# Optimization experiments

Hardware: AMD Instinct MI355X
Metric: run time of the kernel (lower is better)

Reference implementation:

```python
import jax, jax.numpy as jnp
import numpy as np

S, P, D, KH, KW = 1, 1, 1, 3, 3  # stride, padding, dilation, kernel
EPS = 1e-5


def _conv(x, w, b):
    y = jax.lax.conv_general_dilated(
        x, w, (S, S), [(P, P), (P, P)], rhs_dilation=(D, D),
        dimension_numbers=('NCHW', 'OIHW', 'NCHW'))
    return y + b[None, :, None, None]


def _deform_conv(x, offset, mask, w, b):
    # torchvision deform_conv2d v2 semantics: offset layout [B, 2*K, Ho, Wo]
    # with (dy, dx) interleaved per kernel tap; bilinear sampling w/ zero pad.
    B, C, H, W = x.shape
    K = KH * KW
    Ho, Wo = offset.shape[2], offset.shape[3]
    ki, kj = jnp.meshgrid(jnp.arange(KH), jnp.arange(KW), indexing='ij')
    ki = ki.reshape(K).astype(offset.dtype)
    kj = kj.reshape(K).astype(offset.dtype)
    base_y = (jnp.arange(Ho, dtype=offset.dtype) * S - P)[None, None, :, None] + (ki * D)[None, :, None, None]
    base_x = (jnp.arange(Wo, dtype=offset.dtype) * S - P)[None, None, None, :] + (kj * D)[None, :, None, None]
    off = offset.reshape(B, K, 2, Ho, Wo)
    py = base_y + off[:, :, 0]  # [B,K,Ho,Wo]
    px = base_x + off[:, :, 1]
    y0 = jnp.floor(py)
    x0 = jnp.floor(px)
    ly = py - y0
    lx = px - x0
    y0i = y0.astype(jnp.int32)
    x0i = x0.astype(jnp.int32)

    def corner(iy, ix, wgt):
        valid = (iy >= 0) & (iy < H) & (ix >= 0) & (ix < W)
        iyc = jnp.clip(iy, 0, H - 1)
        ixc = jnp.clip(ix, 0, W - 1)
        # gather -> [B, C, K, Ho, Wo]
        v = jax.vmap(lambda img, a, bb: img[:, a, bb])(x, iyc, ixc)
        return v * (wgt * valid)[:, None]

    val = (corner(y0i, x0i, (1 - ly) * (1 - lx))
           + corner(y0i, x0i + 1, (1 - ly) * lx)
           + corner(y0i + 1, x0i, ly * (1 - lx))
           + corner(y0i + 1, x0i + 1, ly * lx))
    val = val * mask[:, None]  # modulation, mask: [B,K,Ho,Wo]
    O = w.shape[0]
    out = jnp.einsum('bckhw,ock->bohw', val, w.reshape(O, C, K))
    return out + b[None, :, None, None]


def setup_inputs() -> dict:
    key = jax.random.key(0)
    ks = jax.random.split(key, 8)
    B, Cin, H, W = 16, 64, 64, 64
    Cout, K = 128, KH * KW
    fan = Cin * K
    x = jax.random.normal(ks[0], (B, Cin, H, W), jnp.float32)
    w_p = jax.random.normal(ks[1], (2 * K, Cin, KH, KW), jnp.float32) * 0.02
    b_p = jax.random.normal(ks[2], (2 * K,), jnp.float32) * 0.01
    w_m = jax.random.normal(ks[3], (K, Cin, KH, KW), jnp.float32) * 0.02
    b_m = jax.random.normal(ks[4], (K,), jnp.float32) * 0.01
    w_d = jax.random.normal(ks[5], (Cout, Cin, KH, KW), jnp.float32) / np.sqrt(fan)
    b_d = jax.random.normal(ks[6], (Cout,), jnp.float32) * 0.01
    gamma = jnp.ones((Cout,), jnp.float32)
    beta = jnp.zeros((Cout,), jnp.float32)
    return {"x": x, "w_p": w_p, "b_p": b_p, "w_m": w_m, "b_m": b_m,
            "w_d": w_d, "b_d": b_d, "gamma": gamma, "beta": beta}


def reference(x, w_p, b_p, w_m, b_m, w_d, b_d, gamma, beta):
    offset = _conv(x, w_p, b_p)                 # [B, 2K, Ho, Wo]
    mask = jax.nn.sigmoid(_conv(x, w_m, b_m))   # [B, K, Ho, Wo]
    y = _deform_conv(x, offset, mask, w_d, b_d)
    # BatchNorm2d (training-mode batch stats, biased variance, eps=1e-5)
    mu = y.mean(axis=(0, 2, 3), keepdims=True)
    var = y.var(axis=(0, 2, 3), keepdims=True)
    yn = (y - mu) * jax.lax.rsqrt(var + EPS)
    yn = yn * gamma[None, :, None, None] + beta[None, :, None, None]
    return jax.nn.gelu(yn, approximate=False)  # nn.GELU default = exact erf
```

## Files before the change

kernel.cpp:

```cpp
#include <hip/hip_runtime.h>
#include <math.h>

#define BB 16
#define CIN 64
#define HH 64
#define WW 64
#define COUT 128
#define HW 4096
#define CK 576
#define CKP 584

typedef __attribute__((ext_vector_type(8))) short short8;
typedef __attribute__((ext_vector_type(4))) float f32x4;

#define WT_OFF    0
#define WPM_OFF   36864
#define XH_OFF    46080
#define SAB_OFF   8434688
#define STAT_OFF  8434944

__device__ __forceinline__ short f2bf(float f) {
    union { float f; unsigned u; } cv; cv.f = f;
    unsigned u = cv.u;
    unsigned r = (u + 0x7fffu + ((u >> 16) & 1u)) >> 16;
    return (short)r;
}
__device__ __forceinline__ float bf2f(short s) {
    union { unsigned u; float f; } cv;
    cv.u = ((unsigned)(unsigned short)s) << 16;
    return cv.f;
}
__device__ __forceinline__ unsigned cvt_pk_bf16(float lo, float hi) {
    unsigned r;
    asm("v_cvt_pk_bf16_f32 %0, %1, %2" : "=v"(r) : "v"(lo), "v"(hi));
    return r;
}

__global__ __launch_bounds__(256) void k_nhwc(const float* __restrict__ x,
                                              short* __restrict__ xh) {
    __shared__ float t[64][65];
    const int blk  = blockIdx.x;
    const int b    = blk >> 6;
    const int pos0 = (blk & 63) << 6;
    const int a    = threadIdx.x & 63;
    const int q    = threadIdx.x >> 6;
#pragma unroll
    for (int i = 0; i < 16; ++i) {
        int c = i * 4 + q;
        t[c][a] = x[((size_t)(b * CIN + c)) * HW + pos0 + a];
    }
    __syncthreads();
#pragma unroll
    for (int i = 0; i < 16; ++i) {
        int p = i * 4 + q;
        xh[((size_t)b * HW + pos0 + p) * CIN + a] = f2bf(t[a][p]);
    }
}

__global__ __launch_bounds__(256) void k_pack(const float* __restrict__ wd,
                                              const float* __restrict__ wp,
                                              const float* __restrict__ wm,
                                              short* __restrict__ wt2,
                                              short* __restrict__ wpm2) {
    int i = blockIdx.x * 256 + threadIdx.x;
    if (i < 18 * 128 * 32) {
        int kc  = i >> 12;
        int rem = i & 4095;
        int co  = rem >> 5;
        int kl  = rem & 31;
        int kk  = kc * 32 + kl;
        int k   = kk >> 6;
        int c   = kk & 63;
        wt2[i] = f2bf(wd[co * CK + c * 9 + k]);
        return;
    }
    i -= 18 * 128 * 32;
    if (i < 18 * 32 * 32) {
        int kc  = i >> 10;
        int rem = i & 1023;
        int t   = rem >> 5;
        int kl  = rem & 31;
        int kk  = kc * 32 + kl;
        int k   = kk >> 6;
        int c   = kk & 63;
        float v = 0.f;
        if (t < 18)      v = wp[t * CK + c * 9 + k];
        else if (t < 27) v = wm[(t - 18) * CK + c * 9 + k];
        wpm2[i] = f2bf(v);
    }
}

__device__ __forceinline__ short8 conv_a(const short* __restrict__ xb,
                                         int ho, int wo, int lk, int kc) {
    const int k  = kc >> 1;
    const int c0 = (kc & 1) * 32 + lk * 8;
    const int yy = ho - 1 + k / 3;
    const int xx = wo - 1 + k % 3;
    const bool valid = ((unsigned)yy < 64u) & ((unsigned)xx < 64u);
    const int yyc = min(max(yy, 0), 63);
    const int xxc = min(max(xx, 0), 63);
    short8 a = *(const short8*)&xb[(((yyc << 6) + xxc) << 6) + c0];
    if (!valid) a = (short8)0;
    return a;
}

#define MPB 32
__global__ __launch_bounds__(512) void k_deform(const short* __restrict__ xh,
                                                const short* __restrict__ wt2,
                                                const short* __restrict__ wpm2,
                                                const float* __restrict__ bp,
                                                const float* __restrict__ bm,
                                                const float* __restrict__ bd,
                                                float* __restrict__ y,
                                                float* __restrict__ gstat) {
    __shared__ short     val[MPB * CKP];
    __shared__ float     s_pm2[2][32][MPB];
    __shared__ unsigned  s_yx[MPB * 9];
    __shared__ _Float16  s_wh[MPB * 9 * 4];

    const int bid  = blockIdx.x;
    const int swz  = (bid & 7) * 256 + (bid >> 3);
    const int pos0 = swz * MPB;
    const int b   = pos0 >> 12;
    const int ho  = (pos0 >> 6) & 63;
    const int wo0 = pos0 & 63;
    const int tid = threadIdx.x;
    const int wv   = tid >> 6;
    const int lane = tid & 63;
    const int l15  = lane & 15;
    const int lk   = lane >> 4;

    const short* xb = xh + (size_t)b * HW * CIN;

    {
        const int mw = wv & 1;
        const int nw = (wv >> 1) & 1;
        const int kh = wv >> 2;
        const int t  = nw * 16 + l15;
        const short* wr = wpm2 + t * 32 + lk * 8;
        const int wo = wo0 + mw * 16 + l15;
        f32x4 acc = (f32x4)(0.f);
#pragma unroll
        for (int kc = kh * 9; kc < kh * 9 + 9; ++kc) {
            short8 a  = conv_a(xb, ho, wo, lk, kc);
            short8 bf = *(const short8*)&wr[kc * 1024];
            acc = __builtin_amdgcn_mfma_f32_16x16x32_bf16(a, bf, acc, 0, 0, 0);
        }
#pragma unroll
        for (int j = 0; j < 4; ++j)
            s_pm2[kh][t][mw * 16 + lk * 4 + j] = acc[j];
    }
    __syncthreads();

    if (tid < MPB * 9) {
        int k = tid >> 5;
        int p = tid & 31;
        int wo = wo0 + p;
        float dy = s_pm2[0][2 * k    ][p] + s_pm2[1][2 * k    ][p] + bp[2 * k];
        float dx = s_pm2[0][2 * k + 1][p] + s_pm2[1][2 * k + 1][p] + bp[2 * k + 1];
        float mm = s_pm2[0][18 + k   ][p] + s_pm2[1][18 + k   ][p] + bm[k];
        float m  = 1.f / (1.f + expf(-mm));
        float py = (float)(ho - 1 + k / 3) + dy;
        float px = (float)(wo - 1 + k % 3) + dx;
        float fy = floorf(py), fx = floorf(px);
        float ly = py - fy, lx = px - fx;
        int y0 = (int)fy, x0 = (int)fx;
        int y1 = y0 + 1, x1 = x0 + 1;
        float vy0 = ((unsigned)y0 < 64u) ? 1.f : 0.f;
        float vy1 = ((unsigned)y1 < 64u) ? 1.f : 0.f;
        float vx0 = ((unsigned)x0 < 64u) ? 1.f : 0.f;
        float vx1 = ((unsigned)x1 < 64u) ? 1.f : 0.f;
        int y0c = min(max(y0, 0), 63), y1c = min(max(y1, 0), 63);
        int x0c = min(max(x0, 0), 63), x1c = min(max(x1, 0), 63);
        int tt = p * 9 + k;
        s_yx[tt] = (unsigned)y0c | ((unsigned)y1c << 8) | ((unsigned)x0c << 16) | ((unsigned)x1c << 24);
        s_wh[tt * 4 + 0] = (_Float16)((1.f - ly) * (1.f - lx) * m * vy0 * vx0);
        s_wh[tt * 4 + 1] = (_Float16)((1.f - ly) * lx * m * vy0 * vx1);
        s_wh[tt * 4 + 2] = (_Float16)(ly * (1.f - lx) * m * vy1 * vx0);
        s_wh[tt * 4 + 3] = (_Float16)(ly * lx * m * vy1 * vx1);
    }
    __syncthreads();

    {
        const int g  = tid >> 3;
        const int li = tid & 7;
        const int c0 = li * 8;
#pragma unroll
        for (int it = 0; it < 5; ++it) {
            int pr = it * 64 + g;
            if (pr < MPB * 9) {
                unsigned yx = s_yx[pr];
                int y0 = yx & 255, y1 = (yx >> 8) & 255;
                int x0 = (yx >> 16) & 255, x1 = yx >> 24;
                float w0 = (float)s_wh[pr * 4 + 0], w1 = (float)s_wh[pr * 4 + 1];
                float w2 = (float)s_wh[pr * 4 + 2], w3 = (float)s_wh[pr * 4 + 3];
                short8 v00 = *(const short8*)&xb[(((y0 << 6) + x0) << 6) + c0];
                short8 v01 = *(const short8*)&xb[(((y0 << 6) + x1) << 6) + c0];
                short8 v10 = *(const short8*)&xb[(((y1 << 6) + x0) << 6) + c0];
                short8 v11 = *(const short8*)&xb[(((y1 << 6) + x1) << 6) + c0];
                int p = pr / 9, k = pr - p * 9;
                union { unsigned u[4]; short8 s; } pk;
#pragma unroll
                for (int h = 0; h < 4; ++h) {
                    float fa = w0 * bf2f(v00[2*h])   + w1 * bf2f(v01[2*h])
                             + w2 * bf2f(v10[2*h])   + w3 * bf2f(v11[2*h]);
                    float fb = w0 * bf2f(v00[2*h+1]) + w1 * bf2f(v01[2*h+1])
                             + w2 * bf2f(v10[2*h+1]) + w3 * bf2f(v11[2*h+1]);
                    pk.u[h] = cvt_pk_bf16(fa, fb);
                }
                *(short8*)&val[p * CKP + (k << 6) + c0] = pk.s;
            }
        }
    }
    __syncthreads();

    f32x4 acc0 = (f32x4)(0.f);
    f32x4 acc1 = (f32x4)(0.f);
    const short* wq = wt2 + (size_t)(wv * 16 + l15) * 32 + lk * 8;
    const int arow = l15 * CKP + lk * 8;
#pragma unroll
    for (int kc = 0; kc < 18; ++kc) {
        short8 a0 = *(const short8*)&val[arow + kc * 32];
        short8 a1 = *(const short8*)&val[arow + 16 * CKP + kc * 32];
        short8 bf = *(const short8*)&wq[kc * 4096];
        acc0 = __builtin_amdgcn_mfma_f32_16x16x32_bf16(a0, bf, acc0, 0, 0, 0);
        acc1 = __builtin_amdgcn_mfma_f32_16x16x32_bf16(a1, bf, acc1, 0, 0, 0);
    }

    const int co = wv * 16 + l15;
    {
        float bias = bd[co];
        float4 o;
        o.x = acc0[0] + bias; o.y = acc0[1] + bias;
        o.z = acc0[2] + bias; o.w = acc0[3] + bias;
        *(float4*)&y[((size_t)(b * COUT + co)) * HW + ho * WW + wo0 + lk * 4] = o;
        o.x = acc1[0] + bias; o.y = acc1[1] + bias;
        o.z = acc1[2] + bias; o.w = acc1[3] + bias;
        *(float4*)&y[((size_t)(b * COUT + co)) * HW + ho * WW + wo0 + 16 + lk * 4] = o;
    }
    float s0 = acc0[0] + acc0[1] + acc0[2] + acc0[3]
             + acc1[0] + acc1[1] + acc1[2] + acc1[3];
    float q0 = acc0[0]*acc0[0] + acc0[1]*acc0[1] + acc0[2]*acc0[2] + acc0[3]*acc0[3]
             + acc1[0]*acc1[0] + acc1[1]*acc1[1] + acc1[2]*acc1[2] + acc1[3]*acc1[3];
    s0 += __shfl_xor(s0, 16); s0 += __shfl_xor(s0, 32);
    q0 += __shfl_xor(q0, 16); q0 += __shfl_xor(q0, 32);
    if (lane < 16) {
        float* slot = gstat + (bid & 63) * 256;
        atomicAdd(&slot[wv * 16 + lane],       s0);
        atomicAdd(&slot[128 + wv * 16 + lane], q0);
    }
}

__global__ __launch_bounds__(128) void k_finalize(const float* __restrict__ gstat,
                                                  const float* __restrict__ bd,
                                                  const float* __restrict__ gamma,
                                                  const float* __restrict__ beta,
                                                  float* __restrict__ sAB) {
    int c = threadIdx.x;
    float s = 0.f, q = 0.f;
    for (int sl = 0; sl < 64; ++sl) {
        s += gstat[sl * 256 + c];
        q += gstat[sl * 256 + 128 + c];
    }
    const float invN = 1.f / (float)(BB * HW);
    float mean_acc = s * invN;
    float var = q * invN - mean_acc * mean_acc;
    float mean_y = mean_acc + bd[c];
    float A = gamma[c] * rsqrtf(var + 1e-5f);
    sAB[c]       = A;
    sAB[128 + c] = beta[c] - mean_y * A;
}

__global__ __launch_bounds__(256) void k_norm_gelu(float* __restrict__ y,
                                                   const float* __restrict__ sAB) {
    int i4 = blockIdx.x * 256 + threadIdx.x;
    if (i4 >= (BB * COUT * HW) / 4) return;
    int c = (i4 >> 10) & 127;
    float A  = sAB[c];
    float Bc = sAB[128 + c];
    float4 v = ((const float4*)y)[i4];
    float4 r;
    float t;
    t = v.x * A + Bc; r.x = 0.5f * t * (1.f + erff(t * 0.70710678118654752f));
    t = v.y * A + Bc; r.y = 0.5f * t * (1.f + erff(t * 0.70710678118654752f));
    t = v.z * A + Bc; r.z = 0.5f * t * (1.f + erff(t * 0.70710678118654752f));
    t = v.w * A + Bc; r.w = 0.5f * t * (1.f + erff(t * 0.70710678118654752f));
    ((float4*)y)[i4] = r;
}

extern "C" void kernel_launch(void* const* d_in, const int* in_sizes, int n_in,
                              void* d_out, int out_size, void* d_ws, size_t ws_size,
                              hipStream_t stream) {
    const float* x     = (const float*)d_in[0];
    const float* w_p   = (const float*)d_in[1];
    const float* b_p   = (const float*)d_in[2];
    const float* w_m   = (const float*)d_in[3];
    const float* b_m   = (const float*)d_in[4];
    const float* w_d   = (const float*)d_in[5];
    const float* b_d   = (const float*)d_in[6];
    const float* gamma = (const float*)d_in[7];
    const float* beta  = (const float*)d_in[8];
    float* ws  = (float*)d_ws;
    float* y   = (float*)d_out;

    short* wt2  = (short*)(ws + WT_OFF);
    short* wpm2 = (short*)(ws + WPM_OFF);
    short* xh   = (short*)(ws + XH_OFF);
    float* sAB  = ws + SAB_OFF;
    float* gstat= ws + STAT_OFF;

    hipMemsetAsync(gstat, 0, 64 * 256 * sizeof(float), stream);
    k_nhwc<<<dim3(1024), dim3(256), 0, stream>>>(x, xh);
    k_pack<<<dim3((18 * 128 * 32 + 18 * 32 * 32) / 256), dim3(256), 0, stream>>>(w_d, w_p, w_m, wt2, wpm2);
    k_deform<<<dim3(BB * HW / MPB), dim3(512), 0, stream>>>(xh, wt2, wpm2, b_p, b_m, b_d, y, gstat);
    k_finalize<<<dim3(1), dim3(128), 0, stream>>>(gstat, b_d, gamma, beta, sAB);
    k_norm_gelu<<<dim3((BB * COUT * HW / 4 + 255) / 256), dim3(256), 0, stream>>>(y, sAB);
}
```

Baseline: 89.90 us.

## Store intermediate conv output in bf16, merge prep kernels, pad LDS rows

The deform kernel now writes its pre-normalization output as bf16 into a workspace buffer instead of fp32 into the output. The norm+GELU pass reads it and writes fp32 to the output, so the intermediate write and re-read move half the bytes. The NHWC transpose and weight packing kernels are merged into one launch. The LDS row layout is padded per kernel tap (68 instead of 64) and the s_pm2 array to 33 columns to cut bank conflicts. BN statistics are still taken from the fp32 accumulators, but the normalized values are computed from bf16-rounded outputs, which adds quantization error.

Result: faster. 86.45 us (-3.8%).

```diff
diff --git a/kernel.cpp b/kernel.cpp
--- a/kernel.cpp
+++ b/kernel.cpp
@@ -8,16 +8,18 @@
 #define COUT 128
 #define HW 4096
 #define CK 576
-#define CKP 584
+#define VROW 612
 
 typedef __attribute__((ext_vector_type(8))) short short8;
+typedef __attribute__((ext_vector_type(4))) short short4v;
 typedef __attribute__((ext_vector_type(4))) float f32x4;
 
 #define WT_OFF    0
 #define WPM_OFF   36864
 #define XH_OFF    46080
-#define SAB_OFF   8434688
-#define STAT_OFF  8434944
+#define YB_OFF    2143232
+#define SAB_OFF   6337536
+#define STAT_OFF  6337792
 
 __device__ __forceinline__ short f2bf(float f) {
     union { float f; unsigned u; } cv; cv.f = f;
@@ -36,33 +38,34 @@
     return r;
 }
 
-__global__ __launch_bounds__(256) void k_nhwc(const float* __restrict__ x,
-                                              short* __restrict__ xh) {
-    __shared__ float t[64][65];
-    const int blk  = blockIdx.x;
-    const int b    = blk >> 6;
-    const int pos0 = (blk & 63) << 6;
-    const int a    = threadIdx.x & 63;
-    const int q    = threadIdx.x >> 6;
-#pragma unroll
-    for (int i = 0; i < 16; ++i) {
-        int c = i * 4 + q;
-        t[c][a] = x[((size_t)(b * CIN + c)) * HW + pos0 + a];
-    }
-    __syncthreads();
-#pragma unroll
-    for (int i = 0; i < 16; ++i) {
-        int p = i * 4 + q;
-        xh[((size_t)b * HW + pos0 + p) * CIN + a] = f2bf(t[a][p]);
-    }
-}
-
-__global__ __launch_bounds__(256) void k_pack(const float* __restrict__ wd,
+__global__ __launch_bounds__(256) void k_prep(const float* __restrict__ x,
+                                              const float* __restrict__ wd,
                                               const float* __restrict__ wp,
                                               const float* __restrict__ wm,
+                                              short* __restrict__ xh,
                                               short* __restrict__ wt2,
                                               short* __restrict__ wpm2) {
-    int i = blockIdx.x * 256 + threadIdx.x;
+    const int blk = blockIdx.x;
+    if (blk < 1024) {
+        __shared__ float t[64][65];
+        const int b    = blk >> 6;
+        const int pos0 = (blk & 63) << 6;
+        const int a    = threadIdx.x & 63;
+        const int q    = threadIdx.x >> 6;
+#pragma unroll
+        for (int i = 0; i < 16; ++i) {
+            int c = i * 4 + q;
+            t[c][a] = x[((size_t)(b * CIN + c)) * HW + pos0 + a];
+        }
+        __syncthreads();
+#pragma unroll
+        for (int i = 0; i < 16; ++i) {
+            int p = i * 4 + q;
+            xh[((size_t)b * HW + pos0 + p) * CIN + a] = f2bf(t[a][p]);
+        }
+        return;
+    }
+    int i = (blk - 1024) * 256 + threadIdx.x;
     if (i < 18 * 128 * 32) {
         int kc  = i >> 12;
         int rem = i & 4095;
@@ -111,10 +114,10 @@
                                                 const float* __restrict__ bp,
                                                 const float* __restrict__ bm,
                                                 const float* __restrict__ bd,
-                                                float* __restrict__ y,
+                                                short* __restrict__ yb,
                                                 float* __restrict__ gstat) {
-    __shared__ short     val[MPB * CKP];
-    __shared__ float     s_pm2[2][32][MPB];
+    __shared__ short     val[MPB * VROW];
+    __shared__ float     s_pm2[2][32][33];
     __shared__ unsigned  s_yx[MPB * 9];
     __shared__ _Float16  s_wh[MPB * 9 * 4];
 
@@ -208,7 +211,7 @@
                              + w2 * bf2f(v10[2*h+1]) + w3 * bf2f(v11[2*h+1]);
                     pk.u[h] = cvt_pk_bf16(fa, fb);
                 }
-                *(short8*)&val[p * CKP + (k << 6) + c0] = pk.s;
+                *(short8*)&val[p * VROW + k * 68 + c0] = pk.s;
             }
         }
     }
@@ -217,11 +220,13 @@
     f32x4 acc0 = (f32x4)(0.f);
     f32x4 acc1 = (f32x4)(0.f);
     const short* wq = wt2 + (size_t)(wv * 16 + l15) * 32 + lk * 8;
-    const int arow = l15 * CKP + lk * 8;
+    const int arow0 = l15 * VROW + lk * 8;
+    const int arow1 = (l15 + 16) * VROW + lk * 8;
 #pragma unroll
     for (int kc = 0; kc < 18; ++kc) {
-        short8 a0 = *(const short8*)&val[arow + kc * 32];
-        short8 a1 = *(const short8*)&val[arow + 16 * CKP + kc * 32];
+        const int koff = (kc >> 1) * 68 + (kc & 1) * 32;
+        short8 a0 = *(const short8*)&val[arow0 + koff];
+        short8 a1 = *(const short8*)&val[arow1 + koff];
         short8 bf = *(const short8*)&wq[kc * 4096];
         acc0 = __builtin_amdgcn_mfma_f32_16x16x32_bf16(a0, bf, acc0, 0, 0, 0);
         acc1 = __builtin_amdgcn_mfma_f32_16x16x32_bf16(a1, bf, acc1, 0, 0, 0);
@@ -230,13 +235,14 @@
     const int co = wv * 16 + l15;
     {
         float bias = bd[co];
-        float4 o;
-        o.x = acc0[0] + bias; o.y = acc0[1] + bias;
-        o.z = acc0[2] + bias; o.w = acc0[3] + bias;
-        *(float4*)&y[((size_t)(b * COUT + co)) * HW + ho * WW + wo0 + lk * 4] = o;
-        o.x = acc1[0] + bias; o.y = acc1[1] + bias;
-        o.z = acc1[2] + bias; o.w = acc1[3] + bias;
-        *(float4*)&y[((size_t)(b * COUT + co)) * HW + ho * WW + wo0 + 16 + lk * 4] = o;
+        short* ybp = yb + ((size_t)(b * COUT + co)) * HW + ho * WW + wo0;
+        union { unsigned u[2]; short4v s; } o0, o1;
+        o0.u[0] = cvt_pk_bf16(acc0[0] + bias, acc0[1] + bias);
+        o0.u[1] = cvt_pk_bf16(acc0[2] + bias, acc0[3] + bias);
+        *(short4v*)&ybp[lk * 4] = o0.s;
+        o1.u[0] = cvt_pk_bf16(acc1[0] + bias, acc1[1] + bias);
+        o1.u[1] = cvt_pk_bf16(acc1[2] + bias, acc1[3] + bias);
+        *(short4v*)&ybp[16 + lk * 4] = o1.s;
     }
     float s0 = acc0[0] + acc0[1] + acc0[2] + acc0[3]
              + acc1[0] + acc1[1] + acc1[2] + acc1[3];
@@ -271,21 +277,27 @@
     sAB[128 + c] = beta[c] - mean_y * A;
 }
 
-__global__ __launch_bounds__(256) void k_norm_gelu(float* __restrict__ y,
-                                                   const float* __restrict__ sAB) {
-    int i4 = blockIdx.x * 256 + threadIdx.x;
-    if (i4 >= (BB * COUT * HW) / 4) return;
-    int c = (i4 >> 10) & 127;
+__global__ __launch_bounds__(256) void k_norm_gelu(const short* __restrict__ yb,
+                                                   const float* __restrict__ sAB,
+                                                   float* __restrict__ out) {
+    int i8 = blockIdx.x * 256 + threadIdx.x;
+    if (i8 >= (BB * COUT * HW) / 8) return;
+    int c = (i8 >> 9) & 127;
     float A  = sAB[c];
     float Bc = sAB[128 + c];
-    float4 v = ((const float4*)y)[i4];
-    float4 r;
+    short8 v = *(const short8*)&yb[(size_t)i8 * 8];
+    float4 r0, r1;
     float t;
-    t = v.x * A + Bc; r.x = 0.5f * t * (1.f + erff(t * 0.70710678118654752f));
-    t = v.y * A + Bc; r.y = 0.5f * t * (1.f + erff(t * 0.70710678118654752f));
-    t = v.z * A + Bc; r.z = 0.5f * t * (1.f + erff(t * 0.70710678118654752f));
-    t = v.w * A + Bc; r.w = 0.5f * t * (1.f + erff(t * 0.70710678118654752f));
-    ((float4*)y)[i4] = r;
+    t = bf2f(v[0]) * A + Bc; r0.x = 0.5f * t * (1.f + erff(t * 0.70710678118654752f));
+    t = bf2f(v[1]) * A + Bc; r0.y = 0.5f * t * (1.f + erff(t * 0.70710678118654752f));
+    t = bf2f(v[2]) * A + Bc; r0.z = 0.5f * t * (1.f + erff(t * 0.70710678118654752f));
+    t = bf2f(v[3]) * A + Bc; r0.w = 0.5f * t * (1.f + erff(t * 0.70710678118654752f));
+    t = bf2f(v[4]) * A + Bc; r1.x = 0.5f * t * (1.f + erff(t * 0.70710678118654752f));
+    t = bf2f(v[5]) * A + Bc; r1.y = 0.5f * t * (1.f + erff(t * 0.70710678118654752f));
+    t = bf2f(v[6]) * A + Bc; r1.z = 0.5f * t * (1.f + erff(t * 0.70710678118654752f));
+    t = bf2f(v[7]) * A + Bc; r1.w = 0.5f * t * (1.f + erff(t * 0.70710678118654752f));
+    *(float4*)&out[(size_t)i8 * 8]     = r0;
+    *(float4*)&out[(size_t)i8 * 8 + 4] = r1;
 }
 
 extern "C" void kernel_launch(void* const* d_in, const int* in_sizes, int n_in,
@@ -301,18 +313,18 @@
     const float* gamma = (const float*)d_in[7];
     const float* beta  = (const float*)d_in[8];
     float* ws  = (float*)d_ws;
-    float* y   = (float*)d_out;
+    float* out = (float*)d_out;
 
     short* wt2  = (short*)(ws + WT_OFF);
     short* wpm2 = (short*)(ws + WPM_OFF);
     short* xh   = (short*)(ws + XH_OFF);
+    short* yb   = (short*)(ws + YB_OFF);
     float* sAB  = ws + SAB_OFF;
     float* gstat= ws + STAT_OFF;
 
     hipMemsetAsync(gstat, 0, 64 * 256 * sizeof(float), stream);
-    k_nhwc<<<dim3(1024), dim3(256), 0, stream>>>(x, xh);
-    k_pack<<<dim3((18 * 128 * 32 + 18 * 32 * 32) / 256), dim3(256), 0, stream>>>(w_d, w_p, w_m, wt2, wpm2);
-    k_deform<<<dim3(BB * HW / MPB), dim3(512), 0, stream>>>(xh, wt2, wpm2, b_p, b_m, b_d, y, gstat);
+    k_prep<<<dim3(1024 + 360), dim3(256), 0, stream>>>(x, w_d, w_p, w_m, xh, wt2, wpm2);
+    k_deform<<<dim3(BB * HW / MPB), dim3(512), 0, stream>>>(xh, wt2, wpm2, b_p, b_m, b_d, yb, gstat);
     k_finalize<<<dim3(1), dim3(128), 0, stream>>>(gstat, b_d, gamma, beta, sAB);
-    k_norm_gelu<<<dim3((BB * COUT * HW / 4 + 255) / 256), dim3(256), 0, stream>>>(y, sAB);
-}
+    k_norm_gelu<<<dim3(BB * COUT * HW / 8 / 256), dim3(256), 0, stream>>>(yb, sAB, out);
+}
```
